# Performance work log

Hardware: AMD Instinct MI355X
Metric: run time of the kernel (lower is better)

## Reference

```python
import jax, jax.numpy as jnp
import numpy as np

B, S, D = 16, 2048, 768
NORM = 1.0 / float(np.sqrt(D))


def setup_inputs() -> dict:
    key = jax.random.key(0)
    k1, k2, k3, k4, k5 = jax.random.split(key, 5)
    b_in = jax.random.normal(k1, (B, S, D), dtype=jnp.float32)
    mask = jax.random.randint(k2, (B, S), 0, 2, dtype=jnp.int64)
    # row 0 must be unmasked: the module returns attention[:, 0, :], and a fully
    # masked query row softmaxes all -inf -> NaN (same quirk as the torch source).
    mask = mask.at[:, 0].set(1)
    Wq = jax.random.normal(k3, (D, D), dtype=jnp.float32) * 0.02
    Wk = jax.random.normal(k4, (D, D), dtype=jnp.float32) * 0.02
    Wv = jax.random.normal(k5, (D, D), dtype=jnp.float32) * 0.02
    return {"b_in": b_in, "mask": mask, "Wq": Wq, "Wk": Wk, "Wv": Wv}


def reference(b_in, mask, Wq, Wk, Wv):
    # nn.Linear(bias=False): y = x @ W.T  (W is [out, in])
    q = jnp.einsum("bsd,ed->bse", b_in, Wq)
    k = jnp.einsum("bsd,ed->bse", b_in, Wk)
    v = jnp.einsum("bsd,ed->bse", b_in, Wv)
    # full [B, S, S] score matrix, as in the original bmm
    scores = jnp.einsum("bqd,bkd->bqk", q, k) * NORM
    # mask.unsqueeze(2): [B, S, 1] broadcasts over the KEY axis -> masks whole query rows
    scores = jnp.where(mask[:, :, None] == 0, -jnp.inf, scores)
    attn = jax.nn.softmax(scores, axis=-1)
    out = jnp.einsum("bqk,bkd->bqd", attn, v)
    return out[:, 0, :]
```

## Files before the change

kernel.cpp:

```cpp
#include <hip/hip_runtime.h>
#include <math.h>

#define BB 16
#define SS 2048
#define DD 768

#define NORM_SCALE 0.036084391824351615f

#define ECH2 16
#define EPC2 (DD / ECH2)

#define RPC 16
#define NCH (SS / RPC)

#define ESEG 8
#define EPB (DD / ESEG)

__global__ void __launch_bounds__(192) qk_fused_kernel(
        const float* __restrict__ x, const float* __restrict__ Wq,
        const float* __restrict__ Wk, float* __restrict__ kq_part) {
    __shared__ float4 xs4[192];
    __shared__ float part[192];
    __shared__ float q0s[EPC2];
    int ec = blockIdx.x;
    int b  = blockIdx.y;
    int t  = threadIdx.x;
    int e0 = ec * EPC2;

    const float4* xr = (const float4*)(x + (size_t)b * SS * DD);
    xs4[t] = xr[t];
    __syncthreads();

    int g = t >> 2, i = t & 3;
    const float4* wq = (const float4*)(Wq + (size_t)(e0 + g) * DD);
    float acc = 0.f;
#pragma unroll 8
    for (int j = 0; j < 48; ++j) {
        float4 xv = xs4[j * 4 + i];
        float4 wv = wq[j * 4 + i];
        acc += xv.x * wv.x + xv.y * wv.y + xv.z * wv.z + xv.w * wv.w;
    }
    part[t] = acc;
    __syncthreads();
    if (t < EPC2)
        q0s[t] = NORM_SCALE *
                 (part[t * 4] + part[t * 4 + 1] + part[t * 4 + 2] + part[t * 4 + 3]);
    __syncthreads();

    const float4* wk = (const float4*)(Wk + (size_t)e0 * DD);
    float4 a = {0.f, 0.f, 0.f, 0.f};
#pragma unroll 4
    for (int e = 0; e < EPC2; ++e) {
        float q  = q0s[e];
        float4 w = wk[e * 192 + t];
        a.x += q * w.x; a.y += q * w.y; a.z += q * w.z; a.w += q * w.w;
    }
    ((float4*)(kq_part + ((size_t)b * ECH2 + ec) * DD))[t] = a;
}

__global__ void __launch_bounds__(64) kq_reduce_kernel(
        const float* __restrict__ kq_part, float* __restrict__ kqs) {
    int b   = blockIdx.x / 3;
    int seg = blockIdx.x % 3;
    int t   = threadIdx.x;
    int idx = seg * 64 + t;
    const float4* kp4 = (const float4*)(kq_part + (size_t)b * ECH2 * DD);
    float4 a = {0.f, 0.f, 0.f, 0.f};
#pragma unroll
    for (int ec = 0; ec < ECH2; ++ec) {
        float4 v = kp4[ec * 192 + idx];
        a.x += v.x; a.y += v.y; a.z += v.z; a.w += v.w;
    }
    ((float4*)(kqs + (size_t)b * DD))[idx] = a;
}

__global__ void __launch_bounds__(256) flash_kernel(
        const float* __restrict__ x,
        const float* __restrict__ kqs,
        float* __restrict__ m_part,
        float* __restrict__ l_part,
        float* __restrict__ o_part) {
    __shared__ float4 osh[4 * 192];
    __shared__ float sc[RPC];
    __shared__ float wsum[4];
    int chunk = blockIdx.x;
    int b     = blockIdx.y;
    int tid   = threadIdx.x;
    int wave  = tid >> 6, lane = tid & 63;
    int s0    = chunk * RPC;

    const float4* xr = (const float4*)(x + ((size_t)b * SS + s0 + wave * 4) * DD);
    float4 xv[12];
#pragma unroll
    for (int j = 0; j < 4; ++j)
#pragma unroll
        for (int k = 0; k < 3; ++k)
            xv[j * 3 + k] = xr[j * (DD / 4) + k * 64 + lane];

    const float4* kr = (const float4*)(kqs + b * DD);
    float4 kf[3];
#pragma unroll
    for (int k = 0; k < 3; ++k) kf[k] = kr[k * 64 + lane];

#pragma unroll
    for (int j = 0; j < 4; ++j) {
        float acc = 0.f;
#pragma unroll
        for (int k = 0; k < 3; ++k) {
            float4 xx = xv[j * 3 + k];
            acc += xx.x * kf[k].x + xx.y * kf[k].y
                 + xx.z * kf[k].z + xx.w * kf[k].w;
        }
#pragma unroll
        for (int off = 32; off > 0; off >>= 1) acc += __shfl_down(acc, off);
        if (lane == 0) sc[wave * 4 + j] = acc;
    }
    __syncthreads();

    float m = sc[0];
#pragma unroll
    for (int r = 1; r < RPC; ++r) m = fmaxf(m, sc[r]);

    float pl = (lane < 4) ? expf(sc[wave * 4 + lane] - m) : 0.f;
    float p0 = __shfl(pl, 0), p1 = __shfl(pl, 1);
    float p2 = __shfl(pl, 2), p3 = __shfl(pl, 3);
    if (lane == 0) wsum[wave] = p0 + p1 + p2 + p3;

#pragma unroll
    for (int k = 0; k < 3; ++k) {
        float4 a;
        a.x = p0 * xv[k].x + p1 * xv[3 + k].x + p2 * xv[6 + k].x + p3 * xv[9 + k].x;
        a.y = p0 * xv[k].y + p1 * xv[3 + k].y + p2 * xv[6 + k].y + p3 * xv[9 + k].y;
        a.z = p0 * xv[k].z + p1 * xv[3 + k].z + p2 * xv[6 + k].z + p3 * xv[9 + k].z;
        a.w = p0 * xv[k].w + p1 * xv[3 + k].w + p2 * xv[6 + k].w + p3 * xv[9 + k].w;
        osh[wave * 192 + k * 64 + lane] = a;
    }
    __syncthreads();

    int pidx = b * NCH + chunk;
    if (tid < 192) {
        float4 s0v = osh[tid], s1 = osh[192 + tid];
        float4 s2 = osh[384 + tid], s3 = osh[576 + tid];
        float4 s;
        s.x = s0v.x + s1.x + s2.x + s3.x;
        s.y = s0v.y + s1.y + s2.y + s3.y;
        s.z = s0v.z + s1.z + s2.z + s3.z;
        s.w = s0v.w + s1.w + s2.w + s3.w;
        ((float4*)(o_part + (size_t)pidx * DD))[tid] = s;
    }
    if (tid == 0) {
        m_part[pidx] = m;
        l_part[pidx] = wsum[0] + wsum[1] + wsum[2] + wsum[3];
    }
}

__global__ void __launch_bounds__(192) combine_out_kernel(
        const float* __restrict__ m_part, const float* __restrict__ l_part,
        const float* __restrict__ o_part, const float* __restrict__ Wv,
        float* __restrict__ out) {
    __shared__ float w[NCH];
    __shared__ float4 c4s[192];
    __shared__ float bc[2];
    int b  = blockIdx.x;
    int es = blockIdx.y;
    int t  = threadIdx.x;

    if (t < 64) {
        float m = fmaxf(m_part[b * NCH + t], m_part[b * NCH + t + 64]);
#pragma unroll
        for (int off = 32; off > 0; off >>= 1) m = fmaxf(m, __shfl_down(m, off));
        if (t == 0) bc[0] = m;
    }
    __syncthreads();
    float M = bc[0];
    if (t < NCH) w[t] = expf(m_part[b * NCH + t] - M);
    __syncthreads();
    if (t < 64) {
        float s = w[t] * l_part[b * NCH + t]
                + w[t + 64] * l_part[b * NCH + t + 64];
#pragma unroll
        for (int off = 32; off > 0; off >>= 1) s += __shfl_down(s, off);
        if (t == 0) bc[1] = 1.f / s;
    }
    __syncthreads();
    float inv = bc[1];

    const float4* op4 = (const float4*)(o_part + (size_t)b * NCH * DD);
    float4 a = {0.f, 0.f, 0.f, 0.f};
#pragma unroll 16
    for (int cc = 0; cc < NCH; ++cc) {
        float4 v = op4[(size_t)cc * 192 + t];
        float ww = w[cc];
        a.x += ww * v.x; a.y += ww * v.y; a.z += ww * v.z; a.w += ww * v.w;
    }
    a.x *= inv; a.y *= inv; a.z *= inv; a.w *= inv;
    c4s[t] = a;
    __syncthreads();

    int r = t >> 1, i = t & 1;
    int e = es * EPB + r;
    const float4* wv = (const float4*)(Wv + (size_t)e * DD);
    float acc = 0.f;
#pragma unroll 8
    for (int j = 0; j < 96; ++j) {
        float4 wvv = wv[j * 2 + i];
        float4 cv  = c4s[j * 2 + i];
        acc += cv.x * wvv.x + cv.y * wvv.y + cv.z * wvv.z + cv.w * wvv.w;
    }
    acc += __shfl_xor(acc, 1);
    if (i == 0) out[b * DD + e] = acc;
}

extern "C" void kernel_launch(void* const* d_in, const int* in_sizes, int n_in,
                              void* d_out, int out_size, void* d_ws, size_t ws_size,
                              hipStream_t stream) {
    const float* b_in = (const float*)d_in[0];
    const float* Wq = (const float*)d_in[2];
    const float* Wk = (const float*)d_in[3];
    const float* Wv = (const float*)d_in[4];
    float* out = (float*)d_out;

    float* ws      = (float*)d_ws;
    float* kq_part = ws;
    float* kqs     = kq_part + (size_t)BB * ECH2 * DD;
    float* m_part  = kqs + BB * DD;
    float* l_part  = m_part + BB * NCH;
    float* o_part  = l_part + BB * NCH;

    qk_fused_kernel<<<dim3(ECH2, BB), 192, 0, stream>>>(b_in, Wq, Wk, kq_part);
    kq_reduce_kernel<<<BB * 3, 64, 0, stream>>>(kq_part, kqs);
    flash_kernel<<<dim3(NCH, BB), 256, 0, stream>>>(b_in, kqs,
                                                    m_part, l_part, o_part);
    combine_out_kernel<<<dim3(BB, ESEG), 192, 0, stream>>>(m_part, l_part,
                                                           o_part, Wv, out);
}
```

Baseline: 189.1 us.

## Split combine and output projection into separate kernels to avoid redundant combine

The fused combine+Wv projection kernel recomputed the full weighted reduction of o_part in every one of its 8 output-segment blocks per batch. The work is now split into a combine kernel that reduces each column once into a workspace buffer, and a separate out-projection kernel that assigns one wavefront per output element. This removes redundant reads of o_part and raises parallelism for the projection. In exchange it adds an extra launch and a round trip through global memory, and the combine kernel uses only 48 blocks with scalar loads.

Result: faster. 183.0 us (-3.2%).

```diff
diff --git a/kernel.cpp b/kernel.cpp
--- a/kernel.cpp
+++ b/kernel.cpp
@@ -12,9 +12,6 @@
 
 #define RPC 16
 #define NCH (SS / RPC)
-
-#define ESEG 8
-#define EPB (DD / ESEG)
 
 __global__ void __launch_bounds__(192) qk_fused_kernel(
         const float* __restrict__ x, const float* __restrict__ Wq,
@@ -154,61 +151,63 @@
     }
 }
 
-__global__ void __launch_bounds__(192) combine_out_kernel(
-        const float* __restrict__ m_part, const float* __restrict__ l_part,
-        const float* __restrict__ o_part, const float* __restrict__ Wv,
-        float* __restrict__ out) {
+__global__ void combine_kernel(const float* __restrict__ m_part,
+                               const float* __restrict__ l_part,
+                               const float* __restrict__ o_part,
+                               float* __restrict__ c) {
     __shared__ float w[NCH];
-    __shared__ float4 c4s[192];
     __shared__ float bc[2];
-    int b  = blockIdx.x;
-    int es = blockIdx.y;
-    int t  = threadIdx.x;
-
-    if (t < 64) {
-        float m = fmaxf(m_part[b * NCH + t], m_part[b * NCH + t + 64]);
+    int b   = blockIdx.x;
+    int seg = blockIdx.y;
+    int tid = threadIdx.x;
+
+    if (tid < 64) {
+        float m = fmaxf(m_part[b * NCH + tid], m_part[b * NCH + tid + 64]);
 #pragma unroll
         for (int off = 32; off > 0; off >>= 1) m = fmaxf(m, __shfl_down(m, off));
-        if (t == 0) bc[0] = m;
+        if (tid == 0) bc[0] = m;
     }
     __syncthreads();
     float M = bc[0];
-    if (t < NCH) w[t] = expf(m_part[b * NCH + t] - M);
-    __syncthreads();
-    if (t < 64) {
-        float s = w[t] * l_part[b * NCH + t]
-                + w[t + 64] * l_part[b * NCH + t + 64];
+    if (tid < NCH) w[tid] = expf(m_part[b * NCH + tid] - M);
+    __syncthreads();
+    if (tid < 64) {
+        float s = w[tid] * l_part[b * NCH + tid]
+                + w[tid + 64] * l_part[b * NCH + tid + 64];
 #pragma unroll
         for (int off = 32; off > 0; off >>= 1) s += __shfl_down(s, off);
-        if (t == 0) bc[1] = 1.f / s;
+        if (tid == 0) bc[1] = 1.f / s;
     }
     __syncthreads();
     float inv = bc[1];
 
-    const float4* op4 = (const float4*)(o_part + (size_t)b * NCH * DD);
-    float4 a = {0.f, 0.f, 0.f, 0.f};
-#pragma unroll 16
-    for (int cc = 0; cc < NCH; ++cc) {
-        float4 v = op4[(size_t)cc * 192 + t];
-        float ww = w[cc];
-        a.x += ww * v.x; a.y += ww * v.y; a.z += ww * v.z; a.w += ww * v.w;
-    }
-    a.x *= inv; a.y *= inv; a.z *= inv; a.w *= inv;
-    c4s[t] = a;
-    __syncthreads();
-
-    int r = t >> 1, i = t & 1;
-    int e = es * EPB + r;
-    const float4* wv = (const float4*)(Wv + (size_t)e * DD);
+    int col = seg * 256 + tid;
+    const float* op = o_part + (size_t)b * NCH * DD + col;
+    float a = 0.f;
+#pragma unroll 8
+    for (int cc = 0; cc < NCH; ++cc) a += w[cc] * op[(size_t)cc * DD];
+    c[b * DD + col] = a * inv;
+}
+
+__global__ void out_proj_kernel(const float* __restrict__ c,
+                                const float* __restrict__ Wv,
+                                float* __restrict__ out) {
+    int wid  = blockIdx.x * 4 + (threadIdx.x >> 6);
+    int lane = threadIdx.x & 63;
+    int b = wid / DD;
+    int e = wid % DD;
+    const float4* xr = (const float4*)(c + (size_t)b * DD);
+    const float4* wr = (const float4*)(Wv + (size_t)e * DD);
     float acc = 0.f;
-#pragma unroll 8
-    for (int j = 0; j < 96; ++j) {
-        float4 wvv = wv[j * 2 + i];
-        float4 cv  = c4s[j * 2 + i];
-        acc += cv.x * wvv.x + cv.y * wvv.y + cv.z * wvv.z + cv.w * wvv.w;
-    }
-    acc += __shfl_xor(acc, 1);
-    if (i == 0) out[b * DD + e] = acc;
+#pragma unroll
+    for (int k = 0; k < 3; ++k) {
+        float4 xv = xr[lane + k * 64];
+        float4 wv = wr[lane + k * 64];
+        acc += xv.x * wv.x + xv.y * wv.y + xv.z * wv.z + xv.w * wv.w;
+    }
+#pragma unroll
+    for (int off = 32; off > 0; off >>= 1) acc += __shfl_down(acc, off);
+    if (lane == 0) out[wid] = acc;
 }
 
 extern "C" void kernel_launch(void* const* d_in, const int* in_sizes, int n_in,
@@ -226,11 +225,12 @@
     float* m_part  = kqs + BB * DD;
     float* l_part  = m_part + BB * NCH;
     float* o_part  = l_part + BB * NCH;
+    float* c       = o_part + (size_t)BB * NCH * DD;
 
     qk_fused_kernel<<<dim3(ECH2, BB), 192, 0, stream>>>(b_in, Wq, Wk, kq_part);
     kq_reduce_kernel<<<BB * 3, 64, 0, stream>>>(kq_part, kqs);
     flash_kernel<<<dim3(NCH, BB), 256, 0, stream>>>(b_in, kqs,
                                                     m_part, l_part, o_part);
-    combine_out_kernel<<<dim3(BB, ESEG), 192, 0, stream>>>(m_part, l_part,
-                                                           o_part, Wv, out);
-}
+    combine_kernel<<<dim3(BB, 3), 256, 0, stream>>>(m_part, l_part, o_part, c);
+    out_proj_kernel<<<BB * DD / 4, 256, 0, stream>>>(c, Wv, out);
+}
```
